# Optimization experiments

Measured on AMD Instinct MI355X. Metric: run time of the kernel, lower is better.

The kernel has to match this reference:

```python
import jax, jax.numpy as jnp
import numpy as np

N, IN, HID, OUT = 18432, 1024, 4096, 4096


def _quantize_per_channel(w):
    # symmetric per-output-channel int8 quantization: scale = max|w|/127
    scale = jnp.max(jnp.abs(w), axis=1) / 127.0  # [rows]
    scale = jnp.maximum(scale, 1e-8)
    w_int8 = jnp.clip(jnp.round(w / scale[:, None]), -127, 127).astype(jnp.int8)
    return w_int8, scale.astype(jnp.float32)


def setup_inputs() -> dict:
    key = jax.random.key(0)
    kx, k1, kb1, k2, kb2 = jax.random.split(key, 5)
    x = jax.random.normal(kx, (N, IN), dtype=jnp.float32)
    # kaiming-uniform-ish float weights, then per-channel int8 quantize
    bound1 = 1.0 / np.sqrt(IN)
    bound2 = 1.0 / np.sqrt(HID)
    w1 = jax.random.uniform(k1, (HID, IN), minval=-bound1, maxval=bound1, dtype=jnp.float32)
    w2 = jax.random.uniform(k2, (OUT, HID), minval=-bound2, maxval=bound2, dtype=jnp.float32)
    w1_int8, w1_scale = _quantize_per_channel(w1)
    w2_int8, w2_scale = _quantize_per_channel(w2)
    b1 = jax.random.uniform(kb1, (HID,), minval=-bound1, maxval=bound1, dtype=jnp.float32)
    b2 = jax.random.uniform(kb2, (OUT,), minval=-bound2, maxval=bound2, dtype=jnp.float32)
    return {"x": x, "w1_int8": w1_int8, "w1_scale": w1_scale, "b1": b1,
            "w2_int8": w2_int8, "w2_scale": w2_scale, "b2": b2}


def reference(x, w1_int8, w1_scale, b1, w2_int8, w2_scale, b2):
    # W8A16 dequant GEMM + fused GELU (layer 1)
    w1 = w1_int8.astype(jnp.float32) * w1_scale[:, None]  # [HID, IN]
    h = jax.nn.gelu(x @ w1.T + b1, approximate=False)      # [N, HID]
    # W8A16 dequant GEMM (layer 2)
    w2 = w2_int8.astype(jnp.float32) * w2_scale[:, None]  # [OUT, HID]
    return h @ w2.T + b2                                   # [N, OUT]
```

## Files before the change

kernel.cpp:

```cpp
#include <hip/hip_runtime.h>
#include <math.h>

#define NROWS 18432
#define IN_DIM 1024
#define HID_DIM 4096
#define OUT_DIM 4096
#define NTN 16

typedef __attribute__((ext_vector_type(8))) short bf16x8;
typedef __attribute__((ext_vector_type(4))) float f32x4;

typedef const __attribute__((address_space(1))) char gchar;
typedef __attribute__((address_space(3))) char lchar;

__device__ __forceinline__ unsigned short f2bf(float f) {
    union { float f; unsigned u; } v; v.f = f;
    unsigned r = v.u + 0x7fffu + ((v.u >> 16) & 1u);
    return (unsigned short)(r >> 16);
}

__device__ __forceinline__ f32x4 MFMA16(bf16x8 a, bf16x8 b, f32x4 c) {
    return __builtin_amdgcn_mfma_f32_16x16x32_bf16(a, b, c, 0, 0, 0);
}


__global__ void cvt_f32_bf16_k(const float4* __restrict__ in, uint4* __restrict__ out, int nvec) {
    int i = blockIdx.x * blockDim.x + threadIdx.x;
    if (i >= nvec) return;
    float4 a = in[2 * i], b = in[2 * i + 1];
    union { unsigned short s[8]; uint4 v; } o;
    o.s[0] = f2bf(a.x); o.s[1] = f2bf(a.y); o.s[2] = f2bf(a.z); o.s[3] = f2bf(a.w);
    o.s[4] = f2bf(b.x); o.s[5] = f2bf(b.y); o.s[6] = f2bf(b.z); o.s[7] = f2bf(b.w);
    out[i] = o.v;
}

__global__ void cvt_i32_bf16_k(const int4* __restrict__ in, uint4* __restrict__ out, int nvec) {
    int i = blockIdx.x * blockDim.x + threadIdx.x;
    if (i >= nvec) return;
    int4 a = in[2 * i], b = in[2 * i + 1];
    union { unsigned short s[8]; uint4 v; } o;
    o.s[0] = f2bf((float)a.x); o.s[1] = f2bf((float)a.y);
    o.s[2] = f2bf((float)a.z); o.s[3] = f2bf((float)a.w);
    o.s[4] = f2bf((float)b.x); o.s[5] = f2bf((float)b.y);
    o.s[6] = f2bf((float)b.z); o.s[7] = f2bf((float)b.w);
    out[i] = o.v;
}

template<int EPI>
__global__ __launch_bounds__(512, 2)
void gemm8q(const unsigned short* __restrict__ A, const unsigned short* __restrict__ B,
            const float* __restrict__ scale, const float* __restrict__ bias,
            void* __restrict__ Cout, int K) {
    extern __shared__ __align__(16) char sm[];

    const int tid  = threadIdx.x;
    const int lane = tid & 63;
    const int wid  = tid >> 6;
    const int wm   = wid >> 2, wn = wid & 3;

    const int nwg  = gridDim.x;
    const int q    = nwg >> 3, r = nwg & 7;
    const int xcd  = blockIdx.x & 7, bidx = blockIdx.x >> 3;
    const int swz  = xcd * q + (xcd < r ? xcd : r) + bidx;
    const int tm   = swz / NTN, tn = swz % NTN;

    const size_t rowbytes = (size_t)K * 2;
    const char* Ag = (const char*)A + (size_t)tm * 256 * rowbytes;
    const char* Bg = (const char*)B + (size_t)tn * 256 * rowbytes;

    const int l16 = lane & 15;
    const int cgi = lane >> 4;
    const int sw  = l16 & 7;
    const int c0  = ((cgi       ^ sw) << 4);
    const int c1  = (((4 | cgi) ^ sw) << 4);

    f32x4  acc[8][4] = {};
    bf16x8 aq[4][2], bn0[2][2], bn1[2][2];

    const int NIT = K >> 7;

#define STAGE(GB, LDSOFF, HR, TILE) { \
    _Pragma("unroll") for (int ld_ = 0; ld_ < 2; ++ld_) { \
        const int po_ = (ld_ << 13) + (tid << 4); \
        const int pr_ = po_ >> 7; \
        const int pc_ = (po_ & 127) ^ ((pr_ & 7) << 4); \
        __builtin_amdgcn_global_load_lds( \
            (gchar*)((GB) + (size_t)((HR) + pr_) * rowbytes + ((size_t)(TILE) << 7) + (size_t)pc_), \
            (lchar*)(sm + (LDSOFF) + po_), 16, 0, 0); \
    } }

#define READ_A(BUFOFF, MH) { const char* Ab_ = sm + (BUFOFF) + wm * 16384; \
    _Pragma("unroll") for (int mm_ = 0; mm_ < 4; ++mm_) { \
        const int ro_ = (((MH) * 64) + mm_ * 16 + l16) << 7; \
        aq[mm_][0] = *(const bf16x8*)(Ab_ + ro_ + c0); \
        aq[mm_][1] = *(const bf16x8*)(Ab_ + ro_ + c1); } }

#define READ_B(BUFOFF, NH, DST) { const char* Bb_ = sm + (BUFOFF) + 32768 + (wn >> 1) * 16384; \
    _Pragma("unroll") for (int nn_ = 0; nn_ < 2; ++nn_) { \
        const int ro_ = (((wn & 1) * 64) + (NH) * 32 + nn_ * 16 + l16) << 7; \
        DST[nn_][0] = *(const bf16x8*)(Bb_ + ro_ + c0); \
        DST[nn_][1] = *(const bf16x8*)(Bb_ + ro_ + c1); } }

#define MF(MH, NH, BQ) { __builtin_amdgcn_s_setprio(1); \
    _Pragma("unroll") for (int mm_ = 0; mm_ < 4; ++mm_) \
        _Pragma("unroll") for (int nn_ = 0; nn_ < 2; ++nn_) { \
            acc[(MH)*4+mm_][(NH)*2+nn_] = MFMA16(aq[mm_][0], BQ[nn_][0], acc[(MH)*4+mm_][(NH)*2+nn_]); \
            acc[(MH)*4+mm_][(NH)*2+nn_] = MFMA16(aq[mm_][1], BQ[nn_][1], acc[(MH)*4+mm_][(NH)*2+nn_]); } \
    __builtin_amdgcn_s_setprio(0); }

#define SFENCE __builtin_amdgcn_sched_barrier(0)
#define WAITV4 { SFENCE; asm volatile("s_waitcnt vmcnt(4)"); SFENCE; }
#define WAITV0 { SFENCE; asm volatile("s_waitcnt vmcnt(0)"); SFENCE; }
#define BARR   { SFENCE; __builtin_amdgcn_s_barrier(); SFENCE; }

    STAGE(Ag, 0,             0,   0); STAGE(Ag, 16384,         128, 0);
    STAGE(Bg, 32768,         0,   0); STAGE(Bg, 49152,         128, 0);
    STAGE(Bg, 65536 + 32768, 0,   1); STAGE(Bg, 65536 + 49152, 128, 1);
    WAITV4; BARR;

    const int NT = K >> 6;
    for (int j = 0; j < NIT; ++j) {
        const int  t0 = 2 * j, t1 = 2 * j + 1;
        const bool p2 = (t0 + 2 < NT);
        const bool p3 = (t1 + 2 < NT);
        const bool lastj = (j == NIT - 1);

        READ_A(0, 0); READ_B(0, 0, bn0);
        STAGE(Ag, 65536, 0, t1);
        BARR; MF(0, 0, bn0);
        READ_B(0, 1, bn1);
        STAGE(Ag, 65536 + 16384, 128, t1);
        BARR; MF(0, 1, bn1);
        READ_A(0, 1);
        if (p2) STAGE(Bg, 32768, 0, t0 + 2);
        BARR; MF(1, 1, bn1);
        if (p2) STAGE(Bg, 49152, 128, t0 + 2);
        if (lastj) { WAITV0; } else { WAITV4; }
        BARR; MF(1, 0, bn0);
        READ_A(65536, 0); READ_B(65536, 0, bn0);
        if (p2) STAGE(Ag, 0, 0, t0 + 2);
        BARR; MF(0, 0, bn0);
        READ_B(65536, 1, bn1);
        if (p2) STAGE(Ag, 16384, 128, t0 + 2);
        BARR; MF(0, 1, bn1);
        READ_A(65536, 1);
        if (p3) STAGE(Bg, 65536 + 32768, 0, t1 + 2);
        BARR; MF(1, 1, bn1);
        if (p3) STAGE(Bg, 65536 + 49152, 128, t1 + 2);
        if (!lastj) { WAITV4; }
        BARR; MF(1, 0, bn0);
    }
#undef STAGE
#undef READ_A
#undef READ_B
#undef MF
#undef SFENCE
#undef WAITV4
#undef WAITV0
#undef BARR

    const int rg = (lane >> 4) << 2;
    #pragma unroll
    for (int nq = 0; nq < 4; ++nq) {
        const int col = tn * 256 + wn * 64 + (nq >> 1) * 32 + (nq & 1) * 16 + l16;
        const float sc = scale[col];
        const float bi = bias[col];
        #pragma unroll
        for (int mq = 0; mq < 8; ++mq) {
            const int row0 = tm * 256 + wm * 128 + (mq >> 2) * 64 + (mq & 3) * 16 + rg;
            #pragma unroll
            for (int rr = 0; rr < 4; ++rr) {
                float v = acc[mq][nq][rr] * sc + bi;
                if (EPI == 0) {
                    float g = 0.5f * v * (1.0f + erff(v * 0.70710678118654752f));
                    ((unsigned short*)Cout)[(size_t)(row0 + rr) * 4096 + col] = f2bf(g);
                } else {
                    ((float*)Cout)[(size_t)(row0 + rr) * 4096 + col] = v;
                }
            }
        }
    }
}

extern "C" void kernel_launch(void* const* d_in, const int* in_sizes, int n_in,
                              void* d_out, int out_size, void* d_ws, size_t ws_size,
                              hipStream_t stream) {
    const float* x   = (const float*)d_in[0];
    const int*   w1q = (const int*)d_in[1];
    const float* s1  = (const float*)d_in[2];
    const float* b1  = (const float*)d_in[3];
    const int*   w2q = (const int*)d_in[4];
    const float* s2  = (const float*)d_in[5];
    const float* b2  = (const float*)d_in[6];
    float*       out = (float*)d_out;

    hipFuncSetAttribute((const void*)gemm8q<0>, hipFuncAttributeMaxDynamicSharedMemorySize, 131072);
    hipFuncSetAttribute((const void*)gemm8q<1>, hipFuncAttributeMaxDynamicSharedMemorySize, 131072);

    char* ws = (char*)d_ws;
    const size_t XBF  = (size_t)NROWS   * IN_DIM  * 2;
    const size_t W1BF = (size_t)HID_DIM * IN_DIM  * 2;
    const size_t W2BF = (size_t)OUT_DIM * HID_DIM * 2;
    const size_t FIXED = XBF + W1BF + W2BF;

    unsigned short* xbf  = (unsigned short*)ws;
    unsigned short* w1bf = (unsigned short*)(ws + XBF);
    unsigned short* w2bf = (unsigned short*)(ws + XBF + W1BF);
    unsigned short* hbuf = (unsigned short*)(ws + FIXED);

    {
        int nvx = NROWS * IN_DIM / 8;
        cvt_f32_bf16_k<<<(nvx + 255) / 256, 256, 0, stream>>>((const float4*)x, (uint4*)xbf, nvx);
        int nv1 = HID_DIM * IN_DIM / 8;
        cvt_i32_bf16_k<<<(nv1 + 255) / 256, 256, 0, stream>>>((const int4*)w1q, (uint4*)w1bf, nv1);
        int nv2 = OUT_DIM * HID_DIM / 8;
        cvt_i32_bf16_k<<<(nv2 + 255) / 256, 256, 0, stream>>>((const int4*)w2q, (uint4*)w2bf, nv2);
    }

    size_t avail = (ws_size > FIXED) ? (ws_size - FIXED) : 0;
    long rp = (long)(avail / ((size_t)HID_DIM * 2));
    rp = (rp / 256) * 256;
    if (rp > NROWS) rp = NROWS;
    if (rp < 256)   rp = 256;

    for (int r0 = 0; r0 < NROWS; r0 += (int)rp) {
        int rows = (int)(((long)(NROWS - r0) < rp) ? (NROWS - r0) : rp);
        dim3 g(NTN * (rows / 256));
        gemm8q<0><<<g, 512, 131072, stream>>>(xbf + (size_t)r0 * IN_DIM, w1bf, s1, b1,
                                              (void*)hbuf, IN_DIM);
        gemm8q<1><<<g, 512, 131072, stream>>>(hbuf, w2bf, s2, b2,
                                              (void*)(out + (size_t)r0 * OUT_DIM), HID_DIM);
    }
    (void)in_sizes; (void)n_in; (void)out_size;
}
```

Baseline: 826.0 us.

## Reschedule GEMM main loop to software-pipeline LDS reads ahead of barriers

```diff
diff --git a/kernel.cpp b/kernel.cpp
--- a/kernel.cpp
+++ b/kernel.cpp
@@ -48,7 +48,7 @@
 
 template<int EPI>
 __global__ __launch_bounds__(512, 2)
-void gemm8q(const unsigned short* __restrict__ A, const unsigned short* __restrict__ B,
+void gemmpl(const unsigned short* __restrict__ A, const unsigned short* __restrict__ B,
             const float* __restrict__ scale, const float* __restrict__ bias,
             void* __restrict__ Cout, int K) {
     extern __shared__ __align__(16) char sm[];
@@ -75,7 +75,7 @@
     const int c1  = (((4 | cgi) ^ sw) << 4);
 
     f32x4  acc[8][4] = {};
-    bf16x8 aq[4][2], bn0[2][2], bn1[2][2];
+    bf16x8 aq[4][2], b0[2][2], b1[2][2];
 
     const int NIT = K >> 7;
 
@@ -109,6 +109,7 @@
     __builtin_amdgcn_s_setprio(0); }
 
 #define SFENCE __builtin_amdgcn_sched_barrier(0)
+#define WAITV2 { SFENCE; asm volatile("s_waitcnt vmcnt(2)"); SFENCE; }
 #define WAITV4 { SFENCE; asm volatile("s_waitcnt vmcnt(4)"); SFENCE; }
 #define WAITV0 { SFENCE; asm volatile("s_waitcnt vmcnt(0)"); SFENCE; }
 #define BARR   { SFENCE; __builtin_amdgcn_s_barrier(); SFENCE; }
@@ -117,44 +118,52 @@
     STAGE(Bg, 32768,         0,   0); STAGE(Bg, 49152,         128, 0);
     STAGE(Bg, 65536 + 32768, 0,   1); STAGE(Bg, 65536 + 49152, 128, 1);
     WAITV4; BARR;
+    READ_A(0, 0); READ_B(0, 0, b0);
 
     const int NT = K >> 6;
     for (int j = 0; j < NIT; ++j) {
-        const int  t0 = 2 * j, t1 = 2 * j + 1;
-        const bool p2 = (t0 + 2 < NT);
-        const bool p3 = (t1 + 2 < NT);
+        const int  tb = 2 * j + 1, tc = 2 * j + 2, td = 2 * j + 3;
         const bool lastj = (j == NIT - 1);
 
-        READ_A(0, 0); READ_B(0, 0, bn0);
-        STAGE(Ag, 65536, 0, t1);
-        BARR; MF(0, 0, bn0);
-        READ_B(0, 1, bn1);
-        STAGE(Ag, 65536 + 16384, 128, t1);
-        BARR; MF(0, 1, bn1);
+        BARR;
+        STAGE(Ag, 65536, 0, tb);
+        MF(0, 0, b0);
+        READ_B(0, 1, b1);
+        BARR;
+        STAGE(Ag, 65536 + 16384, 128, tb);
+        MF(0, 1, b1);
         READ_A(0, 1);
-        if (p2) STAGE(Bg, 32768, 0, t0 + 2);
-        BARR; MF(1, 1, bn1);
-        if (p2) STAGE(Bg, 49152, 128, t0 + 2);
-        if (lastj) { WAITV0; } else { WAITV4; }
-        BARR; MF(1, 0, bn0);
-        READ_A(65536, 0); READ_B(65536, 0, bn0);
-        if (p2) STAGE(Ag, 0, 0, t0 + 2);
-        BARR; MF(0, 0, bn0);
-        READ_B(65536, 1, bn1);
-        if (p2) STAGE(Ag, 16384, 128, t0 + 2);
-        BARR; MF(0, 1, bn1);
+        BARR;
+        if (!lastj) STAGE(Ag, 0, 0, tc);
+        MF(1, 1, b1);
+        if (lastj) { WAITV0; } else { WAITV2; }
+        BARR;
+        if (!lastj) STAGE(Ag, 16384, 128, tc);
+        MF(1, 0, b0);
+        READ_A(65536, 0); READ_B(65536, 0, b0);
+        BARR;
+        if (!lastj) STAGE(Bg, 32768, 0, tc);
+        MF(0, 0, b0);
+        READ_B(65536, 1, b1);
+        BARR;
+        if (!lastj) STAGE(Bg, 49152, 128, tc);
+        MF(0, 1, b1);
         READ_A(65536, 1);
-        if (p3) STAGE(Bg, 65536 + 32768, 0, t1 + 2);
-        BARR; MF(1, 1, bn1);
-        if (p3) STAGE(Bg, 65536 + 49152, 128, t1 + 2);
-        if (!lastj) { WAITV4; }
-        BARR; MF(1, 0, bn0);
+        BARR;
+        if (!lastj) STAGE(Bg, 65536 + 32768, 0, td);
+        MF(1, 1, b1);
+        if (!lastj) { WAITV2; }
+        BARR;
+        if (!lastj) STAGE(Bg, 65536 + 49152, 128, td);
+        MF(1, 0, b0);
+        if (!lastj) { READ_A(0, 0); READ_B(0, 0, b0); }
     }
 #undef STAGE
 #undef READ_A
 #undef READ_B
 #undef MF
 #undef SFENCE
+#undef WAITV2
 #undef WAITV4
 #undef WAITV0
 #undef BARR
@@ -194,8 +203,8 @@
     const float* b2  = (const float*)d_in[6];
     float*       out = (float*)d_out;
 
-    hipFuncSetAttribute((const void*)gemm8q<0>, hipFuncAttributeMaxDynamicSharedMemorySize, 131072);
-    hipFuncSetAttribute((const void*)gemm8q<1>, hipFuncAttributeMaxDynamicSharedMemorySize, 131072);
+    hipFuncSetAttribute((const void*)gemmpl<0>, hipFuncAttributeMaxDynamicSharedMemorySize, 131072);
+    hipFuncSetAttribute((const void*)gemmpl<1>, hipFuncAttributeMaxDynamicSharedMemorySize, 131072);
 
     char* ws = (char*)d_ws;
     const size_t XBF  = (size_t)NROWS   * IN_DIM  * 2;
@@ -226,9 +235,9 @@
     for (int r0 = 0; r0 < NROWS; r0 += (int)rp) {
         int rows = (int)(((long)(NROWS - r0) < rp) ? (NROWS - r0) : rp);
         dim3 g(NTN * (rows / 256));
-        gemm8q<0><<<g, 512, 131072, stream>>>(xbf + (size_t)r0 * IN_DIM, w1bf, s1, b1,
+        gemmpl<0><<<g, 512, 131072, stream>>>(xbf + (size_t)r0 * IN_DIM, w1bf, s1, b1,
                                               (void*)hbuf, IN_DIM);
-        gemm8q<1><<<g, 512, 131072, stream>>>(hbuf, w2bf, s2, b2,
+        gemmpl<1><<<g, 512, 131072, stream>>>(hbuf, w2bf, s2, b2,
                                               (void*)(out + (size_t)r0 * OUT_DIM), HID_DIM);
     }
     (void)in_sizes; (void)n_in; (void)out_size;
```

Result: no change. 827.4 us (+0.2%).

## Shrink GEMM M-tile from 256 to 192 rows to balance CU waves

Applied to the files above, without the earlier changes.

```diff
diff --git a/kernel.cpp b/kernel.cpp
--- a/kernel.cpp
+++ b/kernel.cpp
@@ -6,6 +6,7 @@
 #define HID_DIM 4096
 #define OUT_DIM 4096
 #define NTN 16
+#define BM  192
 
 typedef __attribute__((ext_vector_type(8))) short bf16x8;
 typedef __attribute__((ext_vector_type(4))) float f32x4;
@@ -48,9 +49,9 @@
 
 template<int EPI>
 __global__ __launch_bounds__(512, 2)
-void gemm8q(const unsigned short* __restrict__ A, const unsigned short* __restrict__ B,
-            const float* __restrict__ scale, const float* __restrict__ bias,
-            void* __restrict__ Cout, int K) {
+void gemm192(const unsigned short* __restrict__ A, const unsigned short* __restrict__ B,
+             const float* __restrict__ scale, const float* __restrict__ bias,
+             void* __restrict__ Cout, int K) {
     extern __shared__ __align__(16) char sm[];
 
     const int tid  = threadIdx.x;
@@ -65,7 +66,7 @@
     const int tm   = swz / NTN, tn = swz % NTN;
 
     const size_t rowbytes = (size_t)K * 2;
-    const char* Ag = (const char*)A + (size_t)tm * 256 * rowbytes;
+    const char* Ag = (const char*)A + (size_t)tm * BM * rowbytes;
     const char* Bg = (const char*)B + (size_t)tn * 256 * rowbytes;
 
     const int l16 = lane & 15;
@@ -74,38 +75,37 @@
     const int c0  = ((cgi       ^ sw) << 4);
     const int c1  = (((4 | cgi) ^ sw) << 4);
 
-    f32x4  acc[8][4] = {};
-    bf16x8 aq[4][2], bn0[2][2], bn1[2][2];
+    f32x4  acc[6][4] = {};
+    bf16x8 aq[3][2], bn0[2][2], bn1[2][2];
 
     const int NIT = K >> 7;
 
-#define STAGE(GB, LDSOFF, HR, TILE) { \
-    _Pragma("unroll") for (int ld_ = 0; ld_ < 2; ++ld_) { \
-        const int po_ = (ld_ << 13) + (tid << 4); \
-        const int pr_ = po_ >> 7; \
-        const int pc_ = (po_ & 127) ^ ((pr_ & 7) << 4); \
-        __builtin_amdgcn_global_load_lds( \
-            (gchar*)((GB) + (size_t)((HR) + pr_) * rowbytes + ((size_t)(TILE) << 7) + (size_t)pc_), \
-            (lchar*)(sm + (LDSOFF) + po_), 16, 0, 0); \
-    } }
-
-#define READ_A(BUFOFF, MH) { const char* Ab_ = sm + (BUFOFF) + wm * 16384; \
-    _Pragma("unroll") for (int mm_ = 0; mm_ < 4; ++mm_) { \
-        const int ro_ = (((MH) * 64) + mm_ * 16 + l16) << 7; \
+#define STAGE(GB, LDSOFF, UN, TILE) { \
+    const int po_ = ((UN) << 13) + (tid << 4); \
+    const int pr_ = po_ >> 7; \
+    const int pc_ = (po_ & 127) ^ ((pr_ & 7) << 4); \
+    __builtin_amdgcn_global_load_lds( \
+        (gchar*)((GB) + (size_t)pr_ * rowbytes + ((size_t)(TILE) << 7) + (size_t)pc_), \
+        (lchar*)(sm + (LDSOFF) + po_), 16, 0, 0); \
+}
+
+#define READ_A(BUFOFF, MH) { const char* Ab_ = sm + (BUFOFF); \
+    _Pragma("unroll") for (int mm_ = 0; mm_ < 3; ++mm_) { \
+        const int ro_ = (wm * 96 + (MH) * 48 + mm_ * 16 + l16) << 7; \
         aq[mm_][0] = *(const bf16x8*)(Ab_ + ro_ + c0); \
         aq[mm_][1] = *(const bf16x8*)(Ab_ + ro_ + c1); } }
 
-#define READ_B(BUFOFF, NH, DST) { const char* Bb_ = sm + (BUFOFF) + 32768 + (wn >> 1) * 16384; \
+#define READ_B(BUFOFF, NH, DST) { const char* Bb_ = sm + (BUFOFF) + 24576; \
     _Pragma("unroll") for (int nn_ = 0; nn_ < 2; ++nn_) { \
-        const int ro_ = (((wn & 1) * 64) + (NH) * 32 + nn_ * 16 + l16) << 7; \
+        const int ro_ = ((wn >> 1) * 128 + (wn & 1) * 64 + (NH) * 32 + nn_ * 16 + l16) << 7; \
         DST[nn_][0] = *(const bf16x8*)(Bb_ + ro_ + c0); \
         DST[nn_][1] = *(const bf16x8*)(Bb_ + ro_ + c1); } }
 
 #define MF(MH, NH, BQ) { __builtin_amdgcn_s_setprio(1); \
-    _Pragma("unroll") for (int mm_ = 0; mm_ < 4; ++mm_) \
+    _Pragma("unroll") for (int mm_ = 0; mm_ < 3; ++mm_) \
         _Pragma("unroll") for (int nn_ = 0; nn_ < 2; ++nn_) { \
-            acc[(MH)*4+mm_][(NH)*2+nn_] = MFMA16(aq[mm_][0], BQ[nn_][0], acc[(MH)*4+mm_][(NH)*2+nn_]); \
-            acc[(MH)*4+mm_][(NH)*2+nn_] = MFMA16(aq[mm_][1], BQ[nn_][1], acc[(MH)*4+mm_][(NH)*2+nn_]); } \
+            acc[(MH)*3+mm_][(NH)*2+nn_] = MFMA16(aq[mm_][0], BQ[nn_][0], acc[(MH)*3+mm_][(NH)*2+nn_]); \
+            acc[(MH)*3+mm_][(NH)*2+nn_] = MFMA16(aq[mm_][1], BQ[nn_][1], acc[(MH)*3+mm_][(NH)*2+nn_]); } \
     __builtin_amdgcn_s_setprio(0); }
 
 #define SFENCE __builtin_amdgcn_sched_barrier(0)
@@ -113,41 +113,43 @@
 #define WAITV0 { SFENCE; asm volatile("s_waitcnt vmcnt(0)"); SFENCE; }
 #define BARR   { SFENCE; __builtin_amdgcn_s_barrier(); SFENCE; }
 
-    STAGE(Ag, 0,             0,   0); STAGE(Ag, 16384,         128, 0);
-    STAGE(Bg, 32768,         0,   0); STAGE(Bg, 49152,         128, 0);
-    STAGE(Bg, 65536 + 32768, 0,   1); STAGE(Bg, 65536 + 49152, 128, 1);
+#define BUF1 57344
+
+    STAGE(Ag, 0,            0, 0); STAGE(Ag, 0,            1, 0); STAGE(Ag, 0,            2, 0);
+    STAGE(Bg, 24576,        0, 0); STAGE(Bg, 24576,        1, 0);
+    STAGE(Bg, 24576,        2, 0); STAGE(Bg, 24576,        3, 0);
+    STAGE(Bg, BUF1 + 24576, 0, 1); STAGE(Bg, BUF1 + 24576, 1, 1);
+    STAGE(Bg, BUF1 + 24576, 2, 1); STAGE(Bg, BUF1 + 24576, 3, 1);
     WAITV4; BARR;
 
     const int NT = K >> 6;
     for (int j = 0; j < NIT; ++j) {
         const int  t0 = 2 * j, t1 = 2 * j + 1;
-        const bool p2 = (t0 + 2 < NT);
-        const bool p3 = (t1 + 2 < NT);
         const bool lastj = (j == NIT - 1);
 
         READ_A(0, 0); READ_B(0, 0, bn0);
-        STAGE(Ag, 65536, 0, t1);
+        STAGE(Ag, BUF1, 0, t1); STAGE(Ag, BUF1, 1, t1);
         BARR; MF(0, 0, bn0);
         READ_B(0, 1, bn1);
-        STAGE(Ag, 65536 + 16384, 128, t1);
+        STAGE(Ag, BUF1, 2, t1);
         BARR; MF(0, 1, bn1);
         READ_A(0, 1);
-        if (p2) STAGE(Bg, 32768, 0, t0 + 2);
+        if (!lastj) { STAGE(Bg, 24576, 0, t0 + 2); STAGE(Bg, 24576, 1, t0 + 2); }
         BARR; MF(1, 1, bn1);
-        if (p2) STAGE(Bg, 49152, 128, t0 + 2);
-        if (lastj) { WAITV0; } else { WAITV4; }
+        if (!lastj) { STAGE(Bg, 24576, 2, t0 + 2); STAGE(Bg, 24576, 3, t0 + 2); WAITV4; }
+        else        { WAITV0; }
         BARR; MF(1, 0, bn0);
-        READ_A(65536, 0); READ_B(65536, 0, bn0);
-        if (p2) STAGE(Ag, 0, 0, t0 + 2);
+        READ_A(BUF1, 0); READ_B(BUF1, 0, bn0);
+        if (!lastj) { STAGE(Ag, 0, 0, t0 + 2); STAGE(Ag, 0, 1, t0 + 2); }
         BARR; MF(0, 0, bn0);
-        READ_B(65536, 1, bn1);
-        if (p2) STAGE(Ag, 16384, 128, t0 + 2);
+        READ_B(BUF1, 1, bn1);
+        if (!lastj) STAGE(Ag, 0, 2, t0 + 2);
         BARR; MF(0, 1, bn1);
-        READ_A(65536, 1);
-        if (p3) STAGE(Bg, 65536 + 32768, 0, t1 + 2);
+        READ_A(BUF1, 1);
+        if (!lastj) { STAGE(Bg, BUF1 + 24576, 0, t1 + 2); STAGE(Bg, BUF1 + 24576, 1, t1 + 2); }
         BARR; MF(1, 1, bn1);
-        if (p3) STAGE(Bg, 65536 + 49152, 128, t1 + 2);
-        if (!lastj) { WAITV4; }
+        if (!lastj) { STAGE(Bg, BUF1 + 24576, 2, t1 + 2); STAGE(Bg, BUF1 + 24576, 3, t1 + 2);
+                      WAITV4; }
         BARR; MF(1, 0, bn0);
     }
 #undef STAGE
@@ -158,6 +160,7 @@
 #undef WAITV4
 #undef WAITV0
 #undef BARR
+#undef BUF1
 
     const int rg = (lane >> 4) << 2;
     #pragma unroll
@@ -166,8 +169,8 @@
         const float sc = scale[col];
         const float bi = bias[col];
         #pragma unroll
-        for (int mq = 0; mq < 8; ++mq) {
-            const int row0 = tm * 256 + wm * 128 + (mq >> 2) * 64 + (mq & 3) * 16 + rg;
+        for (int mq = 0; mq < 6; ++mq) {
+            const int row0 = tm * BM + wm * 96 + (mq / 3) * 48 + (mq % 3) * 16 + rg;
             #pragma unroll
             for (int rr = 0; rr < 4; ++rr) {
                 float v = acc[mq][nq][rr] * sc + bi;
@@ -194,8 +197,8 @@
     const float* b2  = (const float*)d_in[6];
     float*       out = (float*)d_out;
 
-    hipFuncSetAttribute((const void*)gemm8q<0>, hipFuncAttributeMaxDynamicSharedMemorySize, 131072);
-    hipFuncSetAttribute((const void*)gemm8q<1>, hipFuncAttributeMaxDynamicSharedMemorySize, 131072);
+    hipFuncSetAttribute((const void*)gemm192<0>, hipFuncAttributeMaxDynamicSharedMemorySize, 114688);
+    hipFuncSetAttribute((const void*)gemm192<1>, hipFuncAttributeMaxDynamicSharedMemorySize, 114688);
 
     char* ws = (char*)d_ws;
     const size_t XBF  = (size_t)NROWS   * IN_DIM  * 2;
@@ -219,17 +222,17 @@
 
     size_t avail = (ws_size > FIXED) ? (ws_size - FIXED) : 0;
     long rp = (long)(avail / ((size_t)HID_DIM * 2));
-    rp = (rp / 256) * 256;
+    rp = (rp / BM) * BM;
     if (rp > NROWS) rp = NROWS;
-    if (rp < 256)   rp = 256;
+    if (rp < BM)    rp = BM;
 
     for (int r0 = 0; r0 < NROWS; r0 += (int)rp) {
         int rows = (int)(((long)(NROWS - r0) < rp) ? (NROWS - r0) : rp);
-        dim3 g(NTN * (rows / 256));
-        gemm8q<0><<<g, 512, 131072, stream>>>(xbf + (size_t)r0 * IN_DIM, w1bf, s1, b1,
-                                              (void*)hbuf, IN_DIM);
-        gemm8q<1><<<g, 512, 131072, stream>>>(hbuf, w2bf, s2, b2,
-                                              (void*)(out + (size_t)r0 * OUT_DIM), HID_DIM);
+        dim3 g(NTN * (rows / BM));
+        gemm192<0><<<g, 512, 114688, stream>>>(xbf + (size_t)r0 * IN_DIM, w1bf, s1, b1,
+                                               (void*)hbuf, IN_DIM);
+        gemm192<1><<<g, 512, 114688, stream>>>(hbuf, w2bf, s2, b2,
+                                               (void*)(out + (size_t)r0 * OUT_DIM), HID_DIM);
     }
     (void)in_sizes; (void)n_in; (void)out_size;
 }
```

After: 801.7 us. -2.9%, faster.
